# Kernel tuning notes

Hardware: AMD Instinct MI355X
Metric: run time of the kernel (lower is better)

## Reference

```python
import jax, jax.numpy as jnp
import numpy as np

B, L, D, H = 32768, 11, 32, 4
HD = D // H
VOCAB, NPOS, PE = 10000, 16, 16
EPS = 1e-5


def _safe_mask(m):
    # disable padding mask for rows where ALL positions are padding
    all_pad = m.all(axis=1)
    return m & ~all_pad[:, None]


def _aggregate(out, query_mask):
    sm = _safe_mask(query_mask)
    valid = (~sm)[..., None].astype(out.dtype)  # (B, L, 1)
    return (out * valid).sum(axis=1) / jnp.clip(valid.sum(axis=1), 1.0, None)


def _mha(xq, xkv, in_w, in_b, out_w, out_b, kpm):
    # torch nn.MultiheadAttention (batch_first, eval): packed in_proj then out_proj
    Bq, Lq, _ = xq.shape
    Wq, Wk, Wv = jnp.split(in_w, 3, axis=0)
    bq, bk, bv = jnp.split(in_b, 3, axis=0)
    q = (xq @ Wq.T + bq).reshape(Bq, Lq, H, HD)
    k = (xkv @ Wk.T + bk).reshape(Bq, -1, H, HD)
    v = (xkv @ Wv.T + bv).reshape(Bq, -1, H, HD)
    s = jnp.einsum('bqhd,bkhd->bhqk', q, k) / np.sqrt(HD).astype(np.float32)
    s = jnp.where(kpm[:, None, None, :], -jnp.inf, s)
    a = jax.nn.softmax(s, axis=-1)
    o = jnp.einsum('bhqk,bkhd->bqhd', a, v).reshape(Bq, Lq, D)
    return o @ out_w.T + out_b


def setup_inputs() -> dict:
    key = jax.random.key(0)
    ks = jax.random.split(key, 14)
    inp = {
        'home_players': jax.random.randint(ks[0], (B, L), 0, VOCAB),
        'away_players': jax.random.randint(ks[1], (B, L), 0, VOCAB),
        'h_positions': jax.random.randint(ks[2], (B, L), 0, NPOS),
        'a_positions': jax.random.randint(ks[3], (B, L), 0, NPOS),
        'emb': jax.random.normal(ks[4], (VOCAB, PE), jnp.float32) * 0.02,
        'pos_emb': jax.random.normal(ks[5], (NPOS, PE), jnp.float32) * 0.02,
        'h2a_in_w': jax.random.normal(ks[6], (3 * D, D), jnp.float32) * 0.05,
        'h2a_in_b': jnp.zeros((3 * D,), jnp.float32),
        'h2a_out_w': jax.random.normal(ks[7], (D, D), jnp.float32) * 0.05,
        'h2a_out_b': jnp.zeros((D,), jnp.float32),
        'a2h_in_w': jax.random.normal(ks[8], (3 * D, D), jnp.float32) * 0.05,
        'a2h_in_b': jnp.zeros((3 * D,), jnp.float32),
        'a2h_out_w': jax.random.normal(ks[9], (D, D), jnp.float32) * 0.05,
        'a2h_out_b': jnp.zeros((D,), jnp.float32),
        'gate_w': jax.random.normal(ks[10], (D, 2 * D), jnp.float32) * 0.05,
        'gate_b': jnp.zeros((D,), jnp.float32),
        'ln_w': jnp.ones((D,), jnp.float32),
        'ln_b': jnp.zeros((D,), jnp.float32),
    }
    return inp


def reference(home_players, away_players, h_positions, a_positions,
              emb, pos_emb,
              h2a_in_w, h2a_in_b, h2a_out_w, h2a_out_b,
              a2h_in_w, a2h_in_b, a2h_out_w, a2h_out_b,
              gate_w, gate_b, ln_w, ln_b):
    h_vecs = jnp.concatenate([emb[home_players], pos_emb[h_positions]], axis=-1)  # (B,L,D)
    a_vecs = jnp.concatenate([emb[away_players], pos_emb[a_positions]], axis=-1)
    h_mask = home_players == 0
    a_mask = away_players == 0
    h2a_out = _mha(h_vecs, a_vecs, h2a_in_w, h2a_in_b, h2a_out_w, h2a_out_b, _safe_mask(a_mask))
    h2a_vec = _aggregate(h2a_out, h_mask)
    a2h_out = _mha(a_vecs, h_vecs, a2h_in_w, a2h_in_b, a2h_out_w, a2h_out_b, _safe_mask(h_mask))
    a2h_vec = _aggregate(a2h_out, a_mask)
    concat = jnp.concatenate([h2a_vec, a2h_vec], axis=1)
    gate = jax.nn.sigmoid(concat @ gate_w.T + gate_b)
    matchup = gate * h2a_vec + (1.0 - gate) * a2h_vec
    mu = matchup.mean(axis=-1, keepdims=True)
    var = ((matchup - mu) ** 2).mean(axis=-1, keepdims=True)
    return (matchup - mu) / jnp.sqrt(var + EPS) * ln_w + ln_b
```

## Files before the change

kernel.cpp:

```cpp
#include <hip/hip_runtime.h>
#include <hip/hip_bf16.h>

typedef unsigned int u32;
typedef unsigned short u16;
typedef short bf16x8 __attribute__((ext_vector_type(8)));
typedef float f32x4 __attribute__((ext_vector_type(4)));
typedef float f32x2 __attribute__((ext_vector_type(2)));

#define LQ 11
#define RPB 8
#define NR 88

#define EMB_OFF   0
#define PEMB_OFF  160000
#define H2AW_OFF  160256
#define A2HW_OFF  163328
#define PACK_N    166400

__device__ __forceinline__ float blo(u32 x) { return __uint_as_float(x << 16); }
__device__ __forceinline__ float bhi(u32 x) { return __uint_as_float(x & 0xFFFF0000u); }
__device__ __forceinline__ float bf1(u16 x) { return __uint_as_float(((u32)x) << 16); }
__device__ __forceinline__ f32x2 kf2(u32 x) { return (f32x2){ blo(x), bhi(x) }; }
__device__ __forceinline__ u16 f2b(float f) {
    __hip_bfloat16 h = __float2bfloat16(f);
    return *reinterpret_cast<u16*>(&h);
}
__device__ __forceinline__ u32 pk2(float a, float b) {
    return (u32)f2b(a) | ((u32)f2b(b) << 16);
}

template<int CTRL>
__device__ __forceinline__ float dppf(float x) {
    return __int_as_float(__builtin_amdgcn_update_dpp(
        0, __float_as_int(x), CTRL, 0xF, 0xF, true));
}
__device__ __forceinline__ float qsum16(float v) {
    v += dppf<0xB1>(v);
    v += dppf<0x4E>(v);
    v += dppf<0x124>(v);
    v += dppf<0x128>(v);
    return v;
}

__global__ __launch_bounds__(256)
void pack_tables(const float* __restrict__ emb, const float* __restrict__ pemb,
                 const float* __restrict__ h2a_w, const float* __restrict__ a2h_w,
                 u16* __restrict__ ws)
{
    const int i = blockIdx.x * 256 + threadIdx.x;
    if (i >= PACK_N) return;
    const float* src; int off;
    if (i < PEMB_OFF)      { src = emb;   off = EMB_OFF; }
    else if (i < H2AW_OFF) { src = pemb;  off = PEMB_OFF; }
    else if (i < A2HW_OFF) { src = h2a_w; off = H2AW_OFF; }
    else                   { src = a2h_w; off = A2HW_OFF; }
    ws[i] = f2b(src[i - off]);
}

__global__ __launch_bounds__(512, 6)
void CrossTeam_v15(const int* __restrict__ home, const int* __restrict__ away,
                   const int* __restrict__ hpos, const int* __restrict__ apos,
                   const u16* __restrict__ wsb,
                   const float* __restrict__ h2a_b,
                   const float* __restrict__ h2a_ow, const float* __restrict__ h2a_ob,
                   const float* __restrict__ a2h_b,
                   const float* __restrict__ a2h_ow, const float* __restrict__ a2h_ob,
                   const float* __restrict__ gw, const float* __restrict__ gb,
                   const float* __restrict__ lnw, const float* __restrict__ lnb,
                   float* __restrict__ out)
{
    __shared__ u16 proj[6][NR * 32];
    __shared__ union {
        int ptab[2][NR][2];
        struct {
            float obuf[2][RPB][32];
            float ybuf[2][RPB][32];
        } cd;
    } u;
    __shared__ u32 mraw[2][RPB];

    const int t = threadIdx.x;
    const int b0 = blockIdx.x * RPB;

    if (t < 176) {
        const int side = t / 88;
        const int s = t - side * 88;
        const int r = s / 11, l = s - r * 11;
        const int gi = (b0 + r) * LQ + l;
        u.ptab[side][s][0] = side ? away[gi] : home[gi];
        u.ptab[side][s][1] = side ? apos[gi] : hpos[gi];
    }
    if (t >= 496) {
        const int k = t - 496; const int side = k >> 3; const int r = k & 7;
        const int* arr = side ? away : home;
        u32 m = 0;
        for (int l = 0; l < LQ; ++l) m |= (u32)(arr[(b0 + r) * LQ + l] == 0) << l;
        mraw[side][r] = m;
    }
    __syncthreads();

    const int wave = t >> 6, lane = t & 63;
    const int lq = lane >> 4, lm = lane & 15;

    {
        const int side = wave >> 2;
        const int mh = (wave >> 1) & 1;
        const int nh = wave & 1;
        const u16* wq_src  = wsb + (side ? A2HW_OFF : H2AW_OFF);
        const u16* wkv_src = wsb + (side ? H2AW_OFF : A2HW_OFF);
        const float* bq_src  = side ? a2h_b : h2a_b;
        const float* bkv_src = side ? h2a_b : a2h_b;
        bf16x8 afrag[3]; float bias[3][4];
        #pragma unroll
        for (int i = 0; i < 3; ++i) {
            const int M = (mh * 3 + i) * 16;
            const u16* wsrc = (M < 32) ? wq_src : wkv_src;
            afrag[i] = *(const bf16x8*)(wsrc + (M + lm) * 32 + lq * 8);
            const float* bs = (M < 32) ? bq_src : bkv_src;
            #pragma unroll
            for (int j = 0; j < 4; ++j) bias[i][j] = bs[M + lq * 4 + j];
        }
        bf16x8 bfrag[3];
        #pragma unroll
        for (int nn = 0; nn < 3; ++nn) {
            const int srow = (nh * 3 + nn) * 16 + lm;
            const int s = srow < NR ? srow : NR - 1;
            const int id = u.ptab[side][s][lq >> 1];
            bfrag[nn] = *(const bf16x8*)
                (wsb + ((lq < 2) ? EMB_OFF : PEMB_OFF) + id * 16 + (lq & 1) * 8);
        }
        #pragma unroll
        for (int nn = 0; nn < 3; ++nn) {
            const int srow = (nh * 3 + nn) * 16 + lm;
            #pragma unroll
            for (int i = 0; i < 3; ++i) {
                f32x4 acc = { bias[i][0], bias[i][1], bias[i][2], bias[i][3] };
                acc = __builtin_amdgcn_mfma_f32_16x16x32_bf16(afrag[i], bfrag[nn], acc, 0, 0, 0);
                const int mt = mh * 3 + i;
                const int mat = side * 3 + (mt >> 1);
                const int dimw = (mt & 1) * 16 + lq * 4;
                if (srow < NR) {
                    const int phys = srow * 32 + ((((dimw >> 3) ^ srow) & 3) << 3) + (dimw & 7);
                    uint2 pk;
                    pk.x = pk2(acc[0], acc[1]);
                    pk.y = pk2(acc[2], acc[3]);
                    *(uint2*)&proj[mat][phys] = pk;
                }
            }
        }
    }
    __syncthreads();

    {
        const int hh = lane >> 4;
        const int slot = lane & 15;
        const int qi = slot < 11 ? slot : 10;
        const int dpv = hh * 8 + (slot & 7);
        #pragma unroll
        for (int it = 0; it < 2; ++it) {
            const int task = wave * 2 + it;
            const int r = task >> 1, dir = task & 1;
            const int qmat = dir ? 3 : 0;
            const int kmat = dir ? 1 : 4;
            const int vmat = dir ? 2 : 5;
            const int r11 = r * 11;
            const u32 kvraw = mraw[dir ? 0 : 1][r];
            const u32 kv = (kvraw == 0x7FFu) ? 0u : kvraw;
            const u32 qraw = mraw[dir ? 1 : 0][r];
            const u32 smq = (qraw == 0x7FFu) ? 0u : qraw;
            const u32 vm = (~smq) & 0x7FFu;
            const float invc = 1.0f / (float)__popc(vm);
            const float wqw = (slot < 11 && ((vm >> slot) & 1u)) ? invc : 0.f;
            const int qrow = r11 + qi;
            const uint4 qp = *(const uint4*)&proj[qmat][qrow * 32 + (((hh ^ qrow) & 3) << 3)];
            const f32x2 sc2 = { 0.35355339059327373f, 0.35355339059327373f };
            f32x2 qv2[4];
            qv2[0] = kf2(qp.x) * sc2; qv2[1] = kf2(qp.y) * sc2;
            qv2[2] = kf2(qp.z) * sc2; qv2[3] = kf2(qp.w) * sc2;
            float e[11]; float sum = 0.f;
            #pragma unroll
            for (int kb = 0; kb < 4; ++kb) {
                const int krow0 = r11 + kb;
                const u16* kbp = &proj[kmat][krow0 * 32 + (((hh ^ krow0) & 3) << 3)];
                #pragma unroll
                for (int m = 0; m < 3; ++m) {
                    const int ki = kb + 4 * m;
                    if (ki < 11) {
                        const uint4 kp = *(const uint4*)(kbp + m * 128);
                        f32x2 acc = qv2[0] * kf2(kp.x);
                        acc += qv2[1] * kf2(kp.y);
                        acc += qv2[2] * kf2(kp.z);
                        acc += qv2[3] * kf2(kp.w);
                        const float s = acc[0] + acc[1];
                        e[ki] = ((kv >> ki) & 1u) ? 0.f : __expf(s);
                        sum += e[ki];
                    }
                }
            }
            const float rs = wqw / fmaxf(sum, 1e-20f);
            float o = 0.f;
            #pragma unroll
            for (int kb = 0; kb < 4; ++kb) {
                const int krow0 = r11 + kb;
                const u16* vbp = &proj[vmat][krow0 * 32 + (((hh ^ krow0) & 3) << 3) + (slot & 7)];
                #pragma unroll
                for (int m = 0; m < 3; ++m) {
                    const int ki = kb + 4 * m;
                    if (ki < 11) {
                        const float v = qsum16(e[ki] * rs);
                        o += v * bf1(vbp[m * 128]);
                    }
                }
            }
            if (slot < 8) u.cd.obuf[dir][r][dpv] = o;
        }
    }
    __syncthreads();

    if (t < 256) {
        const int r = t >> 5, d = t & 31;
        float yh = h2a_ob[d], ya = a2h_ob[d];
        {
            const f32x4* w0 = (const f32x4*)(h2a_ow + d * 32);
            const f32x4* w1 = (const f32x4*)(a2h_ow + d * 32);
            const f32x4* o0 = (const f32x4*)&u.cd.obuf[0][r][0];
            const f32x4* o1 = (const f32x4*)&u.cd.obuf[1][r][0];
            #pragma unroll
            for (int c = 0; c < 8; ++c) {
                const f32x4 a = o0[c], b = w0[c], p = o1[c], q = w1[c];
                yh += a[0]*b[0] + a[1]*b[1] + a[2]*b[2] + a[3]*b[3];
                ya += p[0]*q[0] + p[1]*q[1] + p[2]*q[2] + p[3]*q[3];
            }
        }
        u.cd.ybuf[0][r][d] = yh; u.cd.ybuf[1][r][d] = ya;
        float acc = gb[d];
        {
            const f32x4* g0 = (const f32x4*)(gw + d * 64);
            const f32x4* y0 = (const f32x4*)&u.cd.ybuf[0][r][0];
            const f32x4* y1 = (const f32x4*)&u.cd.ybuf[1][r][0];
            #pragma unroll
            for (int c = 0; c < 8; ++c) {
                const f32x4 a = y0[c], b = g0[c], p = y1[c], q = g0[8 + c];
                acc += a[0]*b[0] + a[1]*b[1] + a[2]*b[2] + a[3]*b[3];
                acc += p[0]*q[0] + p[1]*q[1] + p[2]*q[2] + p[3]*q[3];
            }
        }
        const float g = 1.0f / (1.0f + __expf(-acc));
        const float m = g * yh + (1.0f - g) * ya;
        float s1 = qsum16(m), s2 = qsum16(m * m);
        s1 += __shfl_xor(s1, 16, 32);
        s2 += __shfl_xor(s2, 16, 32);
        const float mu = s1 * 0.03125f;
        const float var = fmaxf(s2 * 0.03125f - mu * mu, 0.f);
        const float res = (m - mu) * rsqrtf(var + 1e-5f) * lnw[d] + lnb[d];
        out[(b0 + r) * 32 + d] = res;
    }
}

__global__ __launch_bounds__(512, 6)
void CrossTeam_v9fb(const int* __restrict__ home, const int* __restrict__ away,
                    const int* __restrict__ hpos, const int* __restrict__ apos,
                    const float* __restrict__ emb, const float* __restrict__ pemb,
                    const float* __restrict__ h2a_w, const float* __restrict__ h2a_b,
                    const float* __restrict__ h2a_ow, const float* __restrict__ h2a_ob,
                    const float* __restrict__ a2h_w, const float* __restrict__ a2h_b,
                    const float* __restrict__ a2h_ow, const float* __restrict__ a2h_ob,
                    const float* __restrict__ gw, const float* __restrict__ gb,
                    const float* __restrict__ lnw, const float* __restrict__ lnb,
                    float* __restrict__ out)
{
    __shared__ u16 proj[6][NR * 32];
    __shared__ union {
        int ptab[2][NR][2];
        struct { float obuf[2][RPB][32]; float ybuf[2][RPB][32]; } cd;
    } u;
    __shared__ u32 mraw[2][RPB];
    const int t = threadIdx.x;
    const int b0 = blockIdx.x * RPB;
    if (t < 176) {
        const int side = t / 88, s = t - side * 88;
        const int r = s / 11, l = s - r * 11;
        const int gi = (b0 + r) * LQ + l;
        u.ptab[side][s][0] = side ? away[gi] : home[gi];
        u.ptab[side][s][1] = side ? apos[gi] : hpos[gi];
    }
    if (t >= 496) {
        const int k = t - 496; const int side = k >> 3; const int r = k & 7;
        const int* arr = side ? away : home;
        u32 m = 0;
        for (int l = 0; l < LQ; ++l) m |= (u32)(arr[(b0 + r) * LQ + l] == 0) << l;
        mraw[side][r] = m;
    }
    __syncthreads();
    const int wave = t >> 6, lane = t & 63;
    const int lq = lane >> 4, lm = lane & 15;
    {
        const int side = wave >> 2, mh = (wave >> 1) & 1, nh = wave & 1;
        const float* wq_src  = side ? a2h_w : h2a_w;
        const float* wkv_src = side ? h2a_w : a2h_w;
        const float* bq_src  = side ? a2h_b : h2a_b;
        const float* bkv_src = side ? h2a_b : a2h_b;
        bf16x8 afrag[3]; float bias[3][4];
        #pragma unroll
        for (int i = 0; i < 3; ++i) {
            const int M = (mh * 3 + i) * 16;
            const float* ws = (M < 32) ? wq_src : wkv_src;
            const float* wp = ws + (M + lm) * 32 + lq * 8;
            const f32x4 a0 = *(const f32x4*)wp;
            const f32x4 a1 = *(const f32x4*)(wp + 4);
            union { bf16x8 v; u32 w[4]; } au;
            au.w[0] = pk2(a0[0], a0[1]); au.w[1] = pk2(a0[2], a0[3]);
            au.w[2] = pk2(a1[0], a1[1]); au.w[3] = pk2(a1[2], a1[3]);
            afrag[i] = au.v;
            const float* bs = (M < 32) ? bq_src : bkv_src;
            #pragma unroll
            for (int j = 0; j < 4; ++j) bias[i][j] = bs[M + lq * 4 + j];
        }
        bf16x8 bfrag[3];
        #pragma unroll
        for (int nn = 0; nn < 3; ++nn) {
            const int srow = (nh * 3 + nn) * 16 + lm;
            const int s = srow < NR ? srow : NR - 1;
            const int id = u.ptab[side][s][lq >> 1];
            const float* gp = ((lq < 2) ? emb : pemb) + id * 16 + (lq & 1) * 8;
            const f32x4 g0 = *(const f32x4*)gp;
            const f32x4 g1 = *(const f32x4*)(gp + 4);
            union { bf16x8 v; u32 w[4]; } bu;
            bu.w[0] = pk2(g0[0], g0[1]); bu.w[1] = pk2(g0[2], g0[3]);
            bu.w[2] = pk2(g1[0], g1[1]); bu.w[3] = pk2(g1[2], g1[3]);
            bfrag[nn] = bu.v;
        }
        #pragma unroll
        for (int nn = 0; nn < 3; ++nn) {
            const int srow = (nh * 3 + nn) * 16 + lm;
            #pragma unroll
            for (int i = 0; i < 3; ++i) {
                f32x4 acc = { bias[i][0], bias[i][1], bias[i][2], bias[i][3] };
                acc = __builtin_amdgcn_mfma_f32_16x16x32_bf16(afrag[i], bfrag[nn], acc, 0, 0, 0);
                const int mt = mh * 3 + i;
                const int mat = side * 3 + (mt >> 1);
                const int dimw = (mt & 1) * 16 + lq * 4;
                if (srow < NR) {
                    const int phys = srow * 32 + ((((dimw >> 3) ^ srow) & 3) << 3) + (dimw & 7);
                    uint2 pk; pk.x = pk2(acc[0], acc[1]); pk.y = pk2(acc[2], acc[3]);
                    *(uint2*)&proj[mat][phys] = pk;
                }
            }
        }
    }
    __syncthreads();
    {
        const int hh = lane >> 4, slot = lane & 15;
        const int qi = slot < 11 ? slot : 10;
        const int dpv = hh * 8 + (slot & 7);
        #pragma unroll
        for (int it = 0; it < 2; ++it) {
            const int task = wave * 2 + it;
            const int r = task >> 1, dir = task & 1;
            const int qmat = dir ? 3 : 0, kmat = dir ? 1 : 4, vmat = dir ? 2 : 5;
            const int r11 = r * 11;
            const u32 kvraw = mraw[dir ? 0 : 1][r];
            const u32 kv = (kvraw == 0x7FFu) ? 0u : kvraw;
            const u32 qraw = mraw[dir ? 1 : 0][r];
            const u32 smq = (qraw == 0x7FFu) ? 0u : qraw;
            const u32 vm = (~smq) & 0x7FFu;
            const float invc = 1.0f / (float)__popc(vm);
            const float wqw = (slot < 11 && ((vm >> slot) & 1u)) ? invc : 0.f;
            const int qrow = r11 + qi;
            const uint4 qp = *(const uint4*)&proj[qmat][qrow * 32 + (((hh ^ qrow) & 3) << 3)];
            float qv[8];
            qv[0]=blo(qp.x); qv[1]=bhi(qp.x); qv[2]=blo(qp.y); qv[3]=bhi(qp.y);
            qv[4]=blo(qp.z); qv[5]=bhi(qp.z); qv[6]=blo(qp.w); qv[7]=bhi(qp.w);
            float e[11]; float sum = 0.f;
            #pragma unroll
            for (int ki = 0; ki < 11; ++ki) {
                const int krow = r11 + ki;
                const uint4 kp = *(const uint4*)&proj[kmat][krow * 32 + (((hh ^ krow) & 3) << 3)];
                float s = qv[0]*blo(kp.x) + qv[1]*bhi(kp.x) + qv[2]*blo(kp.y) + qv[3]*bhi(kp.y)
                        + qv[4]*blo(kp.z) + qv[5]*bhi(kp.z) + qv[6]*blo(kp.w) + qv[7]*bhi(kp.w);
                s *= 0.35355339059327373f;
                e[ki] = ((kv >> ki) & 1u) ? 0.f : __expf(s);
                sum += e[ki];
            }
            const float rs = wqw / fmaxf(sum, 1e-20f);
            float o = 0.f;
            #pragma unroll
            for (int ki = 0; ki < 11; ++ki) {
                float v = e[ki] * rs;
                v += __shfl_xor(v, 1, 16); v += __shfl_xor(v, 2, 16);
                v += __shfl_xor(v, 4, 16); v += __shfl_xor(v, 8, 16);
                const int vrow = r11 + ki;
                o += v * bf1(proj[vmat][vrow * 32 + (((hh ^ vrow) & 3) << 3) + (slot & 7)]);
            }
            if (slot < 8) u.cd.obuf[dir][r][dpv] = o;
        }
    }
    __syncthreads();
    if (t < 256) {
        const int r = t >> 5, d = t & 31;
        float yh = h2a_ob[d];
        const float* wr = h2a_ow + d * 32;
        #pragma unroll
        for (int c = 0; c < 32; ++c) yh += u.cd.obuf[0][r][c] * wr[c];
        float ya = a2h_ob[d];
        wr = a2h_ow + d * 32;
        #pragma unroll
        for (int c = 0; c < 32; ++c) ya += u.cd.obuf[1][r][c] * wr[c];
        u.cd.ybuf[0][r][d] = yh; u.cd.ybuf[1][r][d] = ya;
        float acc = gb[d];
        const float* gr = gw + d * 64;
        #pragma unroll
        for (int c = 0; c < 32; ++c) acc += u.cd.ybuf[0][r][c] * gr[c];
        #pragma unroll
        for (int c = 0; c < 32; ++c) acc += u.cd.ybuf[1][r][c] * gr[32 + c];
        const float g = 1.0f / (1.0f + __expf(-acc));
        const float m = g * yh + (1.0f - g) * ya;
        float s1 = m, s2 = m * m;
        #pragma unroll
        for (int off = 1; off < 32; off <<= 1) {
            s1 += __shfl_xor(s1, off, 32); s2 += __shfl_xor(s2, off, 32);
        }
        const float mu = s1 * 0.03125f;
        const float var = fmaxf(s2 * 0.03125f - mu * mu, 0.f);
        out[(b0 + r) * 32 + d] = (m - mu) * rsqrtf(var + 1e-5f) * lnw[d] + lnb[d];
    }
}

extern "C" void kernel_launch(void* const* d_in, const int* in_sizes, int n_in,
                              void* d_out, int out_size, void* d_ws, size_t ws_size,
                              hipStream_t stream) {
    (void)in_sizes; (void)n_in; (void)out_size;
    if (ws_size >= (size_t)PACK_N * 2) {
        pack_tables<<<(PACK_N + 255) / 256, 256, 0, stream>>>(
            (const float*)d_in[4], (const float*)d_in[5],
            (const float*)d_in[6], (const float*)d_in[10], (u16*)d_ws);
        CrossTeam_v15<<<32768 / RPB, 512, 0, stream>>>(
            (const int*)d_in[0], (const int*)d_in[1], (const int*)d_in[2], (const int*)d_in[3],
            (const u16*)d_ws,
            (const float*)d_in[7], (const float*)d_in[8], (const float*)d_in[9],
            (const float*)d_in[11], (const float*)d_in[12], (const float*)d_in[13],
            (const float*)d_in[14], (const float*)d_in[15], (const float*)d_in[16],
            (const float*)d_in[17], (float*)d_out);
    } else {
        CrossTeam_v9fb<<<32768 / RPB, 512, 0, stream>>>(
            (const int*)d_in[0], (const int*)d_in[1], (const int*)d_in[2], (const int*)d_in[3],
            (const float*)d_in[4], (const float*)d_in[5],
            (const float*)d_in[6], (const float*)d_in[7], (const float*)d_in[8], (const float*)d_in[9],
            (const float*)d_in[10], (const float*)d_in[11], (const float*)d_in[12], (const float*)d_in[13],
            (const float*)d_in[14], (const float*)d_in[15], (const float*)d_in[16], (const float*)d_in[17],
            (float*)d_out);
    }
}
```

Measured before the change: 174.5 us.

## Store Q/K/V projections as fp16, use packed fp16 dot products and exp2

The MFMA output projections are now packed to fp16 instead of bf16. Q is pre-scaled by 1/sqrt(hd)·log2(e), so the score loop can use packed fp16 multiply-adds and a native exp2 in place of fp32 unpack-multiply and __expf. The out-projection and gate dot products are rewritten with two-wide float vectors so they can use packed FMA. Doing the score accumulation in fp16 adds rounding and overflow risk, in exchange for fewer ALU instructions in the attention inner loop.

```diff
diff --git a/kernel.cpp b/kernel.cpp
--- a/kernel.cpp
+++ b/kernel.cpp
@@ -6,6 +6,7 @@
 typedef short bf16x8 __attribute__((ext_vector_type(8)));
 typedef float f32x4 __attribute__((ext_vector_type(4)));
 typedef float f32x2 __attribute__((ext_vector_type(2)));
+typedef _Float16 h16x2 __attribute__((ext_vector_type(2)));
 
 #define LQ 11
 #define RPB 8
@@ -16,6 +17,8 @@
 #define H2AW_OFF  160256
 #define A2HW_OFF  163328
 #define PACK_N    166400
+
+#define QSCALE 0.5100697191248353f
 
 __device__ __forceinline__ float blo(u32 x) { return __uint_as_float(x << 16); }
 __device__ __forceinline__ float bhi(u32 x) { return __uint_as_float(x & 0xFFFF0000u); }
@@ -27,6 +30,21 @@
 }
 __device__ __forceinline__ u32 pk2(float a, float b) {
     return (u32)f2b(a) | ((u32)f2b(b) << 16);
+}
+__device__ __forceinline__ u32 pkh2(float a, float b) {
+    auto h = __builtin_amdgcn_cvt_pkrtz(a, b);
+    return __builtin_bit_cast(u32, h);
+}
+__device__ __forceinline__ h16x2 h2c(u32 x) { return __builtin_bit_cast(h16x2, x); }
+__device__ __forceinline__ float hf1(u16 x) {
+    return (float)__builtin_bit_cast(_Float16, x);
+}
+__device__ __forceinline__ float ex2(float x) {
+#if __has_builtin(__builtin_amdgcn_exp2f)
+    return __builtin_amdgcn_exp2f(x);
+#else
+    return __expf(x * 0.6931471805599453f);
+#endif
 }
 
 template<int CTRL>
@@ -58,7 +76,7 @@
 }
 
 __global__ __launch_bounds__(512, 6)
-void CrossTeam_v15(const int* __restrict__ home, const int* __restrict__ away,
+void CrossTeam_v16(const int* __restrict__ home, const int* __restrict__ away,
                    const int* __restrict__ hpos, const int* __restrict__ apos,
                    const u16* __restrict__ wsb,
                    const float* __restrict__ h2a_b,
@@ -139,11 +157,15 @@
                 const int mt = mh * 3 + i;
                 const int mat = side * 3 + (mt >> 1);
                 const int dimw = (mt & 1) * 16 + lq * 4;
+                if (mt < 2) {
+                    acc[0] *= QSCALE; acc[1] *= QSCALE;
+                    acc[2] *= QSCALE; acc[3] *= QSCALE;
+                }
                 if (srow < NR) {
                     const int phys = srow * 32 + ((((dimw >> 3) ^ srow) & 3) << 3) + (dimw & 7);
                     uint2 pk;
-                    pk.x = pk2(acc[0], acc[1]);
-                    pk.y = pk2(acc[2], acc[3]);
+                    pk.x = pkh2(acc[0], acc[1]);
+                    pk.y = pkh2(acc[2], acc[3]);
                     *(uint2*)&proj[mat][phys] = pk;
                 }
             }
@@ -173,10 +195,7 @@
             const float wqw = (slot < 11 && ((vm >> slot) & 1u)) ? invc : 0.f;
             const int qrow = r11 + qi;
             const uint4 qp = *(const uint4*)&proj[qmat][qrow * 32 + (((hh ^ qrow) & 3) << 3)];
-            const f32x2 sc2 = { 0.35355339059327373f, 0.35355339059327373f };
-            f32x2 qv2[4];
-            qv2[0] = kf2(qp.x) * sc2; qv2[1] = kf2(qp.y) * sc2;
-            qv2[2] = kf2(qp.z) * sc2; qv2[3] = kf2(qp.w) * sc2;
+            const h16x2 q0 = h2c(qp.x), q1 = h2c(qp.y), q2 = h2c(qp.z), q3 = h2c(qp.w);
             float e[11]; float sum = 0.f;
             #pragma unroll
             for (int kb = 0; kb < 4; ++kb) {
@@ -187,12 +206,12 @@
                     const int ki = kb + 4 * m;
                     if (ki < 11) {
                         const uint4 kp = *(const uint4*)(kbp + m * 128);
-                        f32x2 acc = qv2[0] * kf2(kp.x);
-                        acc += qv2[1] * kf2(kp.y);
-                        acc += qv2[2] * kf2(kp.z);
-                        acc += qv2[3] * kf2(kp.w);
-                        const float s = acc[0] + acc[1];
-                        e[ki] = ((kv >> ki) & 1u) ? 0.f : __expf(s);
+                        h16x2 a2 = q0 * h2c(kp.x);
+                        a2 += q1 * h2c(kp.y);
+                        a2 += q2 * h2c(kp.z);
+                        a2 += q3 * h2c(kp.w);
+                        const float s = (float)(a2[0] + a2[1]);
+                        e[ki] = ((kv >> ki) & 1u) ? 0.f : ex2(s);
                         sum += e[ki];
                     }
                 }
@@ -208,7 +227,7 @@
                     const int ki = kb + 4 * m;
                     if (ki < 11) {
                         const float v = qsum16(e[ki] * rs);
-                        o += v * bf1(vbp[m * 128]);
+                        o += v * hf1(vbp[m * 128]);
                     }
                 }
             }
@@ -219,7 +238,8 @@
 
     if (t < 256) {
         const int r = t >> 5, d = t & 31;
-        float yh = h2a_ob[d], ya = a2h_ob[d];
+        f32x2 sh = {0.f, 0.f}, sh2 = {0.f, 0.f};
+        f32x2 sa = {0.f, 0.f}, sa2 = {0.f, 0.f};
         {
             const f32x4* w0 = (const f32x4*)(h2a_ow + d * 32);
             const f32x4* w1 = (const f32x4*)(a2h_ow + d * 32);
@@ -228,12 +248,16 @@
             #pragma unroll
             for (int c = 0; c < 8; ++c) {
                 const f32x4 a = o0[c], b = w0[c], p = o1[c], q = w1[c];
-                yh += a[0]*b[0] + a[1]*b[1] + a[2]*b[2] + a[3]*b[3];
-                ya += p[0]*q[0] + p[1]*q[1] + p[2]*q[2] + p[3]*q[3];
-            }
-        }
+                sh  += (f32x2){a[0], a[1]} * (f32x2){b[0], b[1]};
+                sh2 += (f32x2){a[2], a[3]} * (f32x2){b[2], b[3]};
+                sa  += (f32x2){p[0], p[1]} * (f32x2){q[0], q[1]};
+                sa2 += (f32x2){p[2], p[3]} * (f32x2){q[2], q[3]};
+            }
+        }
+        const float yh = h2a_ob[d] + (sh[0] + sh[1]) + (sh2[0] + sh2[1]);
+        const float ya = a2h_ob[d] + (sa[0] + sa[1]) + (sa2[0] + sa2[1]);
         u.cd.ybuf[0][r][d] = yh; u.cd.ybuf[1][r][d] = ya;
-        float acc = gb[d];
+        f32x2 g1 = {0.f, 0.f}, g2 = {0.f, 0.f};
         {
             const f32x4* g0 = (const f32x4*)(gw + d * 64);
             const f32x4* y0 = (const f32x4*)&u.cd.ybuf[0][r][0];
@@ -241,10 +265,13 @@
             #pragma unroll
             for (int c = 0; c < 8; ++c) {
                 const f32x4 a = y0[c], b = g0[c], p = y1[c], q = g0[8 + c];
-                acc += a[0]*b[0] + a[1]*b[1] + a[2]*b[2] + a[3]*b[3];
-                acc += p[0]*q[0] + p[1]*q[1] + p[2]*q[2] + p[3]*q[3];
-            }
-        }
+                g1 += (f32x2){a[0], a[1]} * (f32x2){b[0], b[1]};
+                g1 += (f32x2){a[2], a[3]} * (f32x2){b[2], b[3]};
+                g2 += (f32x2){p[0], p[1]} * (f32x2){q[0], q[1]};
+                g2 += (f32x2){p[2], p[3]} * (f32x2){q[2], q[3]};
+            }
+        }
+        const float acc = gb[d] + (g1[0] + g1[1]) + (g2[0] + g2[1]);
         const float g = 1.0f / (1.0f + __expf(-acc));
         const float m = g * yh + (1.0f - g) * ya;
         float s1 = qsum16(m), s2 = qsum16(m * m);
@@ -434,7 +461,7 @@
         pack_tables<<<(PACK_N + 255) / 256, 256, 0, stream>>>(
             (const float*)d_in[4], (const float*)d_in[5],
             (const float*)d_in[6], (const float*)d_in[10], (u16*)d_ws);
-        CrossTeam_v15<<<32768 / RPB, 512, 0, stream>>>(
+        CrossTeam_v16<<<32768 / RPB, 512, 0, stream>>>(
             (const int*)d_in[0], (const int*)d_in[1], (const int*)d_in[2], (const int*)d_in[3],
             (const u16*)d_ws,
             (const float*)d_in[7], (const float*)d_in[8], (const float*)d_in[9],
```

After: 172.1 us. Within noise of the previous version (-1.4%).
